# Kernel tuning notes

Hardware: AMD Instinct MI355X
Metric: run time of the kernel (lower is better)

Reference implementation:

```python
import jax, jax.numpy as jnp
import numpy as np


def setup_inputs() -> dict:
    key = jax.random.key(0)
    k0, k1, k2, k3 = jax.random.split(key, 4)
    B, S, D, F, E = 2, 2048, 1024, 4096, 8
    hidden_states = jax.random.normal(k0, (B, S, D), dtype=jnp.float32)
    Wr = jax.random.normal(k1, (E, D), dtype=jnp.float32) * 0.02   # router Linear weight [E, D]
    W1 = jax.random.normal(k2, (E, D, F), dtype=jnp.float32) * 0.02  # expert w1 (transposed torch layout)
    W2 = jax.random.normal(k3, (E, F, D), dtype=jnp.float32) * 0.02  # expert w2
    return {"hidden_states": hidden_states, "Wr": Wr, "W1": W1, "W2": W2, "top_k": 2}


def reference(hidden_states, Wr, W1, W2, top_k):
    # hidden_states: [B, S, D]; Wr: [E, D]; W1: [E, D, F]; W2: [E, F, D]
    E = Wr.shape[0]
    dt = hidden_states.dtype

    # Router: logits -> top-k expert indices. NOTE: the original module computes
    # softmax routing weights over the top-k logits but never applies them in the
    # combine step, so the output is an UNWEIGHTED sum over selected experts.
    router_logits = jnp.einsum('bsd,ed->bse', hidden_states, Wr)
    _, topk_idx = jax.lax.top_k(router_logits, top_k)            # [B, S, K]

    # mask[b,s,e] = 1 if expert e is in token (b,s)'s top-k (indices are distinct)
    mask = (jax.nn.one_hot(topk_idx, E, dtype=dt).sum(axis=-2) > 0).astype(dt)  # [B, S, E]

    # Dense per-expert FFN (SiLU MLP, no bias, dropout=identity in eval):
    h = jax.nn.silu(jnp.einsum('bsd,edf->bsef', hidden_states, W1))  # [B, S, E, F]
    y = jnp.einsum('bsef,efd->bsed', h, W2)                          # [B, S, E, D]

    # Combine: unweighted sum over selected experts (faithful to source)
    return jnp.einsum('bsed,bse->bsd', y, mask)
```

## Files before the change

### kernel.cpp

```cpp
#include <hip/hip_runtime.h>
#include <hip/hip_bf16.h>
#include <stdint.h>

#define TOKENS 4096
#define DDIM 1024
#define FDIM 4096
#define NEXP 8
#define BM 128
#define BN 128
#define BK2 32

typedef __attribute__((ext_vector_type(4))) float f32x4;
typedef __attribute__((ext_vector_type(8))) short short8;

__device__ __forceinline__ unsigned short f2bf(float f) {
    union { float f; uint32_t u; } v; v.f = f;
    uint32_t u = v.u;
    return (unsigned short)((u + 0x7fff + ((u >> 16) & 1)) >> 16);
}

#define BARRIER() asm volatile("s_barrier" ::: "memory")
#define WAIT_VM0() asm volatile("s_waitcnt vmcnt(0)" ::: "memory")
#define WAIT_VM4() asm volatile("s_waitcnt vmcnt(4)" ::: "memory")
#define WAIT_LGKM0() asm volatile("s_waitcnt lgkmcnt(0)" ::: "memory")
#define GLDS(SRC, DST) __builtin_amdgcn_global_load_lds( \
    (const __attribute__((address_space(1))) void*)(SRC), \
    (__attribute__((address_space(3))) void*)(DST), 16, 0, 0)

__device__ __forceinline__ short8 dsr(uint32_t addr) {
    short8 d;
    asm volatile("ds_read_b128 %0, %1" : "=v"(d) : "v"(addr));
    return d;
}

__global__ __launch_bounds__(256) void cvt_x(const float* __restrict__ x,
                                             unsigned short* __restrict__ xb, int n) {
    int i = (blockIdx.x * 256 + threadIdx.x) * 8;
    if (i >= n) return;
    float4 a = *(const float4*)(x + i);
    float4 b = *(const float4*)(x + i + 4);
    short8 o;
    o[0] = f2bf(a.x); o[1] = f2bf(a.y); o[2] = f2bf(a.z); o[3] = f2bf(a.w);
    o[4] = f2bf(b.x); o[5] = f2bf(b.y); o[6] = f2bf(b.z); o[7] = f2bf(b.w);
    *(short8*)(xb + i) = o;
}

__global__ __launch_bounds__(256) void transpose_cvt(const float* __restrict__ in,
                                                     unsigned short* __restrict__ out,
                                                     int R, int C) {
    __shared__ float tile[32][33];
    int e = blockIdx.z;
    int r0 = blockIdx.y * 32, c0 = blockIdx.x * 32;
    const float* src = in + (size_t)e * R * C;
    unsigned short* dst = out + (size_t)e * R * C;
    int t = threadIdx.x;
    int rr = t >> 3;
    int cc = (t & 7) * 4;
    float4 v = *(const float4*)(src + (size_t)(r0 + rr) * C + c0 + cc);
    tile[rr][cc + 0] = v.x; tile[rr][cc + 1] = v.y;
    tile[rr][cc + 2] = v.z; tile[rr][cc + 3] = v.w;
    __syncthreads();
    int oc = rr;
    int orr = cc;
    ushort4 o;
    o.x = f2bf(tile[orr + 0][oc]);
    o.y = f2bf(tile[orr + 1][oc]);
    o.z = f2bf(tile[orr + 2][oc]);
    o.w = f2bf(tile[orr + 3][oc]);
    *(ushort4*)(dst + (size_t)(c0 + oc) * R + r0 + orr) = o;
}

__global__ __launch_bounds__(256) void router(const float* __restrict__ x,
                                              const float* __restrict__ wr,
                                              int* __restrict__ cnt,
                                              int* __restrict__ list) {
    __shared__ float wl[NEXP * DDIM];
    int t = threadIdx.x;
    for (int i = t; i < NEXP * DDIM; i += 256) wl[i] = wr[i];
    __syncthreads();
    int tok = blockIdx.x * 4 + (t >> 6);
    int lane = t & 63;
    float acc[NEXP];
#pragma unroll
    for (int e = 0; e < NEXP; e++) acc[e] = 0.f;
    const float* xr = x + (size_t)tok * DDIM;
    for (int d = lane; d < DDIM; d += 64) {
        float xv = xr[d];
#pragma unroll
        for (int e = 0; e < NEXP; e++) acc[e] += xv * wl[e * DDIM + d];
    }
#pragma unroll
    for (int e = 0; e < NEXP; e++) {
#pragma unroll
        for (int off = 32; off; off >>= 1) acc[e] += __shfl_xor(acc[e], off);
    }
    if (lane == 0) {
        int e1 = 0; float v1 = acc[0];
        for (int e = 1; e < NEXP; e++) if (acc[e] > v1) { v1 = acc[e]; e1 = e; }
        int e2 = -1; float v2 = -1e30f;
        for (int e = 0; e < NEXP; e++) if (e != e1 && acc[e] > v2) { v2 = acc[e]; e2 = e; }
        int p1 = atomicAdd(&cnt[e1], 1);
        list[e1 * TOKENS + p1] = tok;
        int p2 = atomicAdd(&cnt[e2], 1);
        list[e2 * TOKENS + p2] = tok;
    }
}

__global__ void setup(const int* __restrict__ cnt, int* __restrict__ off,
                      int* __restrict__ wbA, int* __restrict__ wbB,
                      int* __restrict__ qctr) {
    if (threadIdx.x == 0) {
        int s = 0, ta = 0, tb = 0;
        for (int e = 0; e < NEXP; e++) {
            off[e] = s; s += cnt[e];
            wbA[e] = ta; wbB[e] = tb;
            int ntm = (cnt[e] + BM - 1) / BM;
            ta += ntm * (FDIM / BN);
            tb += ntm * (DDIM / BN) * 2;
        }
        wbA[NEXP] = ta; wbB[NEXP] = tb;
        qctr[0] = 0; qctr[1] = 0;
    }
}

template <bool GATHER_A, bool SILU, int KSPLIT>
__global__ __launch_bounds__(256, 3) void gemm_moe8(
    const unsigned short* __restrict__ Abase,
    const unsigned short* __restrict__ Wt,
    const int* __restrict__ cnt, const int* __restrict__ off,
    const int* __restrict__ list,
    const int* __restrict__ wbase,
    int* __restrict__ qctr,
    unsigned short* __restrict__ Hout,
    float* __restrict__ Yout,
    int KD, int KLEN, int NW) {
    __shared__ alignas(16) unsigned short As[3][BM * BK2];
    __shared__ alignas(16) unsigned short Bs[3][BN * BK2];
    __shared__ int wsh;

    const int t = threadIdx.x;
    const int lane = t & 63;
    const int wid = t >> 6;
    const int wm = wid >> 1, wn = wid & 1;
    const int r16 = lane & 15, g = lane >> 4;
    const int total = wbase[NEXP];

    const uint32_t asB = (uint32_t)(uintptr_t)&As[0][0];
    const uint32_t bsB = (uint32_t)(uintptr_t)&Bs[0][0];
    uint32_t aAdr[4], bAdr[4];
#pragma unroll
    for (int mi = 0; mi < 4; mi++) {
        int row = wm * 64 + mi * 16 + r16;
        aAdr[mi] = asB + row * 64 + ((g ^ ((row >> 1) & 3)) << 4);
    }
#pragma unroll
    for (int nj = 0; nj < 4; nj++) {
        int row = wn * 64 + nj * 16 + r16;
        bAdr[nj] = bsB + row * 64 + ((g ^ ((row >> 1) & 3)) << 4);
    }

    for (;;) {
        if (t == 0) wsh = atomicAdd(qctr, 1);
        __syncthreads();
        int w = wsh;
        if (w >= total) break;

        int e = 0;
        while (e < NEXP - 1 && w >= wbase[e + 1]) e++;
        w -= wbase[e];
        const int n_e = cnt[e];
        const int ntm = (n_e + BM - 1) >> 7;
        int idx = w / ntm;
        const int mtile = w - idx * ntm;
        int kc = 0;
        if (KSPLIT == 2) { kc = idx & 1; idx >>= 1; }
        const int m0 = mtile * BM;
        const int n0 = idx * BN;
        const int base = off[e];
        const int k0 = kc * KLEN;

        const unsigned short* pA[2];
        const unsigned short* pB[2];
        int ldsOff[2];
#pragma unroll
        for (int i = 0; i < 2; i++) {
            int c = i * 256 + t;
            int row = c >> 2, p = c & 3;
            int cg = p ^ ((row >> 1) & 3);
            int arow = m0 + row; if (arow >= n_e) arow = n_e - 1;
            size_t grow = GATHER_A ? (size_t)list[e * TOKENS + arow] : (size_t)(base + arow);
            pA[i] = Abase + grow * (size_t)KD + k0 + (cg << 3);
            pB[i] = Wt + ((size_t)e * NW + n0 + row) * (size_t)KD + k0 + (cg << 3);
            ldsOff[i] = c * 16;
        }

        f32x4 acc[4][4];
#pragma unroll
        for (int i = 0; i < 4; i++)
#pragma unroll
            for (int j = 0; j < 4; j++) acc[i][j] = f32x4{0.f, 0.f, 0.f, 0.f};

#pragma unroll
        for (int s = 0; s < 2; ++s) {
#pragma unroll
            for (int i = 0; i < 2; i++) { GLDS(pA[i], (char*)As[s] + ldsOff[i]); pA[i] += BK2; }
#pragma unroll
            for (int i = 0; i < 2; i++) { GLDS(pB[i], (char*)Bs[s] + ldsOff[i]); pB[i] += BK2; }
        }
        WAIT_VM4();
        BARRIER();

        uint32_t o0 = 0, o1 = 8192, o2 = 16384;

        const int NT = KLEN / BK2;
        for (int tk = 0; tk < NT; ++tk) {
            if (tk + 2 < NT) {
#pragma unroll
                for (int i = 0; i < 2; i++) { GLDS(pA[i], (char*)As[0] + o2 + ldsOff[i]); pA[i] += BK2; }
#pragma unroll
                for (int i = 0; i < 2; i++) { GLDS(pB[i], (char*)Bs[0] + o2 + ldsOff[i]); pB[i] += BK2; }
            }

            short8 a0 = dsr(aAdr[0] + o0);
            short8 a1 = dsr(aAdr[1] + o0);
            short8 a2 = dsr(aAdr[2] + o0);
            short8 a3 = dsr(aAdr[3] + o0);
            short8 b0 = dsr(bAdr[0] + o0);
            short8 b1 = dsr(bAdr[1] + o0);
            short8 b2 = dsr(bAdr[2] + o0);
            short8 b3 = dsr(bAdr[3] + o0);
            WAIT_LGKM0();
            __builtin_amdgcn_sched_barrier(0);

            __builtin_amdgcn_s_setprio(1);
            acc[0][0] = __builtin_amdgcn_mfma_f32_16x16x32_bf16(a0, b0, acc[0][0], 0, 0, 0);
            acc[0][1] = __builtin_amdgcn_mfma_f32_16x16x32_bf16(a0, b1, acc[0][1], 0, 0, 0);
            acc[0][2] = __builtin_amdgcn_mfma_f32_16x16x32_bf16(a0, b2, acc[0][2], 0, 0, 0);
            acc[0][3] = __builtin_amdgcn_mfma_f32_16x16x32_bf16(a0, b3, acc[0][3], 0, 0, 0);
            acc[1][0] = __builtin_amdgcn_mfma_f32_16x16x32_bf16(a1, b0, acc[1][0], 0, 0, 0);
            acc[1][1] = __builtin_amdgcn_mfma_f32_16x16x32_bf16(a1, b1, acc[1][1], 0, 0, 0);
            acc[1][2] = __builtin_amdgcn_mfma_f32_16x16x32_bf16(a1, b2, acc[1][2], 0, 0, 0);
            acc[1][3] = __builtin_amdgcn_mfma_f32_16x16x32_bf16(a1, b3, acc[1][3], 0, 0, 0);
            acc[2][0] = __builtin_amdgcn_mfma_f32_16x16x32_bf16(a2, b0, acc[2][0], 0, 0, 0);
            acc[2][1] = __builtin_amdgcn_mfma_f32_16x16x32_bf16(a2, b1, acc[2][1], 0, 0, 0);
            acc[2][2] = __builtin_amdgcn_mfma_f32_16x16x32_bf16(a2, b2, acc[2][2], 0, 0, 0);
            acc[2][3] = __builtin_amdgcn_mfma_f32_16x16x32_bf16(a2, b3, acc[2][3], 0, 0, 0);
            acc[3][0] = __builtin_amdgcn_mfma_f32_16x16x32_bf16(a3, b0, acc[3][0], 0, 0, 0);
            acc[3][1] = __builtin_amdgcn_mfma_f32_16x16x32_bf16(a3, b1, acc[3][1], 0, 0, 0);
            acc[3][2] = __builtin_amdgcn_mfma_f32_16x16x32_bf16(a3, b2, acc[3][2], 0, 0, 0);
            acc[3][3] = __builtin_amdgcn_mfma_f32_16x16x32_bf16(a3, b3, acc[3][3], 0, 0, 0);
            __builtin_amdgcn_s_setprio(0);

            if (tk + 1 < NT) {
                if (tk + 2 < NT) WAIT_VM4();
                else             WAIT_VM0();
                BARRIER();
            }
            uint32_t tmp = o0; o0 = o1; o1 = o2; o2 = tmp;
        }

#pragma unroll
        for (int mi = 0; mi < 4; ++mi) {
#pragma unroll
            for (int nj = 0; nj < 4; ++nj) {
#pragma unroll
                for (int qq = 0; qq < 4; ++qq) {
                    int lr = wm * 64 + mi * 16 + g * 4 + qq;
                    if (m0 + lr < n_e) {
                        int col = n0 + wn * 64 + nj * 16 + r16;
                        float v = acc[mi][nj][qq];
                        if (SILU) {
                            v = v / (1.f + __expf(-v));
                            Hout[(size_t)(base + m0 + lr) * NW + col] = f2bf(v);
                        } else {
                            int tok = list[e * TOKENS + m0 + lr];
                            atomicAdd(&Yout[(size_t)tok * NW + col], v);
                        }
                    }
                }
            }
        }
    }
}

extern "C" void kernel_launch(void* const* d_in, const int* in_sizes, int n_in,
                              void* d_out, int out_size, void* d_ws, size_t ws_size,
                              hipStream_t stream) {
    const float* X  = (const float*)d_in[0];
    const float* Wr = (const float*)d_in[1];
    const float* W1 = (const float*)d_in[2];
    const float* W2 = (const float*)d_in[3];
    float* Y = (float*)d_out;

    char* ws = (char*)d_ws;
    int* cnt  = (int*)(ws + 0);
    int* off  = (int*)(ws + 64);
    int* wbA  = (int*)(ws + 128);
    int* wbB  = (int*)(ws + 192);
    int* qctr = (int*)(ws + 256);
    int* list = (int*)(ws + 1024);
    unsigned short* Xb = (unsigned short*)(ws + (1ull << 20));
    unsigned short* WT = (unsigned short*)(ws + (16ull << 20));
    unsigned short* H  = (unsigned short*)(ws + (80ull << 20));

    hipMemsetAsync(d_out, 0, (size_t)out_size * sizeof(float), stream);
    hipMemsetAsync(cnt, 0, 32, stream);

    cvt_x<<<TOKENS * DDIM / (256 * 8), 256, 0, stream>>>(X, Xb, TOKENS * DDIM);
    router<<<TOKENS / 4, 256, 0, stream>>>(X, Wr, cnt, list);
    setup<<<1, 64, 0, stream>>>(cnt, off, wbA, wbB, qctr);

    transpose_cvt<<<dim3(FDIM / 32, DDIM / 32, NEXP), 256, 0, stream>>>(W1, WT, DDIM, FDIM);
    gemm_moe8<true, true, 1><<<768, 256, 0, stream>>>(
        Xb, WT, cnt, off, list, wbA, qctr + 0, H, nullptr, DDIM, DDIM, FDIM);

    transpose_cvt<<<dim3(DDIM / 32, FDIM / 32, NEXP), 256, 0, stream>>>(W2, WT, FDIM, DDIM);
    gemm_moe8<false, false, 2><<<768, 256, 0, stream>>>(
        H, WT, cnt, off, list, wbB, qctr + 1, nullptr, Y, FDIM, FDIM / 2, DDIM);
}
```

Before: 463.1 us.

## Enlarge MoE GEMM tiles to 256x256 with 512-thread blocks and 4-way K split

Doubles the GEMM block tile in both M and N to 256x256, using 8 waves per block, each computing a 128x64 sub-tile with 8x4 MFMA accumulators. The block's A and B tiles are shared across more waves, so the intent is higher arithmetic intensity per LDS and global load. The second GEMM moves from a 2-way to a 4-way K split to keep enough work items. The costs are more registers per wave, fewer resident blocks per CU, more padding waste for expert token counts that are not multiples of 256, and more atomic adds into the output.

```diff
diff --git a/kernel.cpp b/kernel.cpp
--- a/kernel.cpp
+++ b/kernel.cpp
@@ -6,8 +6,8 @@
 #define DDIM 1024
 #define FDIM 4096
 #define NEXP 8
-#define BM 128
-#define BN 128
+#define BM 256
+#define BN 256
 #define BK2 32
 
 typedef __attribute__((ext_vector_type(4))) float f32x4;
@@ -114,9 +114,9 @@
         for (int e = 0; e < NEXP; e++) {
             off[e] = s; s += cnt[e];
             wbA[e] = ta; wbB[e] = tb;
-            int ntm = (cnt[e] + BM - 1) / BM;
+            int ntm = (cnt[e] + BM - 1) >> 8;
             ta += ntm * (FDIM / BN);
-            tb += ntm * (DDIM / BN) * 2;
+            tb += ntm * (DDIM / BN) * 4;
         }
         wbA[NEXP] = ta; wbB[NEXP] = tb;
         qctr[0] = 0; qctr[1] = 0;
@@ -124,7 +124,7 @@
 }
 
 template <bool GATHER_A, bool SILU, int KSPLIT>
-__global__ __launch_bounds__(256, 3) void gemm_moe8(
+__global__ __launch_bounds__(512, 2) void gemm_moe15(
     const unsigned short* __restrict__ Abase,
     const unsigned short* __restrict__ Wt,
     const int* __restrict__ cnt, const int* __restrict__ off,
@@ -141,16 +141,16 @@
     const int t = threadIdx.x;
     const int lane = t & 63;
     const int wid = t >> 6;
-    const int wm = wid >> 1, wn = wid & 1;
+    const int wm = wid >> 2, wn = wid & 3;
     const int r16 = lane & 15, g = lane >> 4;
     const int total = wbase[NEXP];
 
     const uint32_t asB = (uint32_t)(uintptr_t)&As[0][0];
     const uint32_t bsB = (uint32_t)(uintptr_t)&Bs[0][0];
-    uint32_t aAdr[4], bAdr[4];
-#pragma unroll
-    for (int mi = 0; mi < 4; mi++) {
-        int row = wm * 64 + mi * 16 + r16;
+    uint32_t aAdr[8], bAdr[4];
+#pragma unroll
+    for (int mi = 0; mi < 8; mi++) {
+        int row = wm * 128 + mi * 16 + r16;
         aAdr[mi] = asB + row * 64 + ((g ^ ((row >> 1) & 3)) << 4);
     }
 #pragma unroll
@@ -169,11 +169,11 @@
         while (e < NEXP - 1 && w >= wbase[e + 1]) e++;
         w -= wbase[e];
         const int n_e = cnt[e];
-        const int ntm = (n_e + BM - 1) >> 7;
-        int idx = w / ntm;
-        const int mtile = w - idx * ntm;
-        int kc = 0;
-        if (KSPLIT == 2) { kc = idx & 1; idx >>= 1; }
+        const int ntm = (n_e + BM - 1) >> 8;
+        int combined = w / ntm;
+        const int mtile = w - combined * ntm;
+        const int kc = (KSPLIT > 1) ? (combined & (KSPLIT - 1)) : 0;
+        const int idx = (KSPLIT > 1) ? (combined / KSPLIT) : combined;
         const int m0 = mtile * BM;
         const int n0 = idx * BN;
         const int base = off[e];
@@ -184,7 +184,7 @@
         int ldsOff[2];
 #pragma unroll
         for (int i = 0; i < 2; i++) {
-            int c = i * 256 + t;
+            int c = i * 512 + t;
             int row = c >> 2, p = c & 3;
             int cg = p ^ ((row >> 1) & 3);
             int arow = m0 + row; if (arow >= n_e) arow = n_e - 1;
@@ -194,9 +194,9 @@
             ldsOff[i] = c * 16;
         }
 
-        f32x4 acc[4][4];
-#pragma unroll
-        for (int i = 0; i < 4; i++)
+        f32x4 acc[8][4];
+#pragma unroll
+        for (int i = 0; i < 8; i++)
 #pragma unroll
             for (int j = 0; j < 4; j++) acc[i][j] = f32x4{0.f, 0.f, 0.f, 0.f};
 
@@ -210,7 +210,7 @@
         WAIT_VM4();
         BARRIER();
 
-        uint32_t o0 = 0, o1 = 8192, o2 = 16384;
+        uint32_t o0 = 0, o1 = 16384, o2 = 32768;
 
         const int NT = KLEN / BK2;
         for (int tk = 0; tk < NT; ++tk) {
@@ -221,35 +221,63 @@
                 for (int i = 0; i < 2; i++) { GLDS(pB[i], (char*)Bs[0] + o2 + ldsOff[i]); pB[i] += BK2; }
             }
 
-            short8 a0 = dsr(aAdr[0] + o0);
-            short8 a1 = dsr(aAdr[1] + o0);
-            short8 a2 = dsr(aAdr[2] + o0);
-            short8 a3 = dsr(aAdr[3] + o0);
-            short8 b0 = dsr(bAdr[0] + o0);
-            short8 b1 = dsr(bAdr[1] + o0);
-            short8 b2 = dsr(bAdr[2] + o0);
-            short8 b3 = dsr(bAdr[3] + o0);
-            WAIT_LGKM0();
-            __builtin_amdgcn_sched_barrier(0);
-
-            __builtin_amdgcn_s_setprio(1);
-            acc[0][0] = __builtin_amdgcn_mfma_f32_16x16x32_bf16(a0, b0, acc[0][0], 0, 0, 0);
-            acc[0][1] = __builtin_amdgcn_mfma_f32_16x16x32_bf16(a0, b1, acc[0][1], 0, 0, 0);
-            acc[0][2] = __builtin_amdgcn_mfma_f32_16x16x32_bf16(a0, b2, acc[0][2], 0, 0, 0);
-            acc[0][3] = __builtin_amdgcn_mfma_f32_16x16x32_bf16(a0, b3, acc[0][3], 0, 0, 0);
-            acc[1][0] = __builtin_amdgcn_mfma_f32_16x16x32_bf16(a1, b0, acc[1][0], 0, 0, 0);
-            acc[1][1] = __builtin_amdgcn_mfma_f32_16x16x32_bf16(a1, b1, acc[1][1], 0, 0, 0);
-            acc[1][2] = __builtin_amdgcn_mfma_f32_16x16x32_bf16(a1, b2, acc[1][2], 0, 0, 0);
-            acc[1][3] = __builtin_amdgcn_mfma_f32_16x16x32_bf16(a1, b3, acc[1][3], 0, 0, 0);
-            acc[2][0] = __builtin_amdgcn_mfma_f32_16x16x32_bf16(a2, b0, acc[2][0], 0, 0, 0);
-            acc[2][1] = __builtin_amdgcn_mfma_f32_16x16x32_bf16(a2, b1, acc[2][1], 0, 0, 0);
-            acc[2][2] = __builtin_amdgcn_mfma_f32_16x16x32_bf16(a2, b2, acc[2][2], 0, 0, 0);
-            acc[2][3] = __builtin_amdgcn_mfma_f32_16x16x32_bf16(a2, b3, acc[2][3], 0, 0, 0);
-            acc[3][0] = __builtin_amdgcn_mfma_f32_16x16x32_bf16(a3, b0, acc[3][0], 0, 0, 0);
-            acc[3][1] = __builtin_amdgcn_mfma_f32_16x16x32_bf16(a3, b1, acc[3][1], 0, 0, 0);
-            acc[3][2] = __builtin_amdgcn_mfma_f32_16x16x32_bf16(a3, b2, acc[3][2], 0, 0, 0);
-            acc[3][3] = __builtin_amdgcn_mfma_f32_16x16x32_bf16(a3, b3, acc[3][3], 0, 0, 0);
-            __builtin_amdgcn_s_setprio(0);
+            {
+                short8 b0 = dsr(bAdr[0] + o0);
+                short8 b1 = dsr(bAdr[1] + o0);
+                short8 b2 = dsr(bAdr[2] + o0);
+                short8 b3 = dsr(bAdr[3] + o0);
+                short8 a0 = dsr(aAdr[0] + o0);
+                short8 a1 = dsr(aAdr[1] + o0);
+                short8 a2 = dsr(aAdr[2] + o0);
+                short8 a3 = dsr(aAdr[3] + o0);
+                WAIT_LGKM0();
+                __builtin_amdgcn_sched_barrier(0);
+
+                __builtin_amdgcn_s_setprio(1);
+                acc[0][0] = __builtin_amdgcn_mfma_f32_16x16x32_bf16(a0, b0, acc[0][0], 0, 0, 0);
+                acc[0][1] = __builtin_amdgcn_mfma_f32_16x16x32_bf16(a0, b1, acc[0][1], 0, 0, 0);
+                acc[0][2] = __builtin_amdgcn_mfma_f32_16x16x32_bf16(a0, b2, acc[0][2], 0, 0, 0);
+                acc[0][3] = __builtin_amdgcn_mfma_f32_16x16x32_bf16(a0, b3, acc[0][3], 0, 0, 0);
+                acc[1][0] = __builtin_amdgcn_mfma_f32_16x16x32_bf16(a1, b0, acc[1][0], 0, 0, 0);
+                acc[1][1] = __builtin_amdgcn_mfma_f32_16x16x32_bf16(a1, b1, acc[1][1], 0, 0, 0);
+                acc[1][2] = __builtin_amdgcn_mfma_f32_16x16x32_bf16(a1, b2, acc[1][2], 0, 0, 0);
+                acc[1][3] = __builtin_amdgcn_mfma_f32_16x16x32_bf16(a1, b3, acc[1][3], 0, 0, 0);
+                acc[2][0] = __builtin_amdgcn_mfma_f32_16x16x32_bf16(a2, b0, acc[2][0], 0, 0, 0);
+                acc[2][1] = __builtin_amdgcn_mfma_f32_16x16x32_bf16(a2, b1, acc[2][1], 0, 0, 0);
+                acc[2][2] = __builtin_amdgcn_mfma_f32_16x16x32_bf16(a2, b2, acc[2][2], 0, 0, 0);
+                acc[2][3] = __builtin_amdgcn_mfma_f32_16x16x32_bf16(a2, b3, acc[2][3], 0, 0, 0);
+                acc[3][0] = __builtin_amdgcn_mfma_f32_16x16x32_bf16(a3, b0, acc[3][0], 0, 0, 0);
+                acc[3][1] = __builtin_amdgcn_mfma_f32_16x16x32_bf16(a3, b1, acc[3][1], 0, 0, 0);
+                acc[3][2] = __builtin_amdgcn_mfma_f32_16x16x32_bf16(a3, b2, acc[3][2], 0, 0, 0);
+                acc[3][3] = __builtin_amdgcn_mfma_f32_16x16x32_bf16(a3, b3, acc[3][3], 0, 0, 0);
+                __builtin_amdgcn_s_setprio(0);
+
+                short8 a4 = dsr(aAdr[4] + o0);
+                short8 a5 = dsr(aAdr[5] + o0);
+                short8 a6 = dsr(aAdr[6] + o0);
+                short8 a7 = dsr(aAdr[7] + o0);
+                WAIT_LGKM0();
+                __builtin_amdgcn_sched_barrier(0);
+
+                __builtin_amdgcn_s_setprio(1);
+                acc[4][0] = __builtin_amdgcn_mfma_f32_16x16x32_bf16(a4, b0, acc[4][0], 0, 0, 0);
+                acc[4][1] = __builtin_amdgcn_mfma_f32_16x16x32_bf16(a4, b1, acc[4][1], 0, 0, 0);
+                acc[4][2] = __builtin_amdgcn_mfma_f32_16x16x32_bf16(a4, b2, acc[4][2], 0, 0, 0);
+                acc[4][3] = __builtin_amdgcn_mfma_f32_16x16x32_bf16(a4, b3, acc[4][3], 0, 0, 0);
+                acc[5][0] = __builtin_amdgcn_mfma_f32_16x16x32_bf16(a5, b0, acc[5][0], 0, 0, 0);
+                acc[5][1] = __builtin_amdgcn_mfma_f32_16x16x32_bf16(a5, b1, acc[5][1], 0, 0, 0);
+                acc[5][2] = __builtin_amdgcn_mfma_f32_16x16x32_bf16(a5, b2, acc[5][2], 0, 0, 0);
+                acc[5][3] = __builtin_amdgcn_mfma_f32_16x16x32_bf16(a5, b3, acc[5][3], 0, 0, 0);
+                acc[6][0] = __builtin_amdgcn_mfma_f32_16x16x32_bf16(a6, b0, acc[6][0], 0, 0, 0);
+                acc[6][1] = __builtin_amdgcn_mfma_f32_16x16x32_bf16(a6, b1, acc[6][1], 0, 0, 0);
+                acc[6][2] = __builtin_amdgcn_mfma_f32_16x16x32_bf16(a6, b2, acc[6][2], 0, 0, 0);
+                acc[6][3] = __builtin_amdgcn_mfma_f32_16x16x32_bf16(a6, b3, acc[6][3], 0, 0, 0);
+                acc[7][0] = __builtin_amdgcn_mfma_f32_16x16x32_bf16(a7, b0, acc[7][0], 0, 0, 0);
+                acc[7][1] = __builtin_amdgcn_mfma_f32_16x16x32_bf16(a7, b1, acc[7][1], 0, 0, 0);
+                acc[7][2] = __builtin_amdgcn_mfma_f32_16x16x32_bf16(a7, b2, acc[7][2], 0, 0, 0);
+                acc[7][3] = __builtin_amdgcn_mfma_f32_16x16x32_bf16(a7, b3, acc[7][3], 0, 0, 0);
+                __builtin_amdgcn_s_setprio(0);
+            }
 
             if (tk + 1 < NT) {
                 if (tk + 2 < NT) WAIT_VM4();
@@ -260,12 +288,12 @@
         }
 
 #pragma unroll
-        for (int mi = 0; mi < 4; ++mi) {
+        for (int mi = 0; mi < 8; ++mi) {
 #pragma unroll
             for (int nj = 0; nj < 4; ++nj) {
 #pragma unroll
                 for (int qq = 0; qq < 4; ++qq) {
-                    int lr = wm * 64 + mi * 16 + g * 4 + qq;
+                    int lr = wm * 128 + mi * 16 + g * 4 + qq;
                     if (m0 + lr < n_e) {
                         int col = n0 + wn * 64 + nj * 16 + r16;
                         float v = acc[mi][nj][qq];
@@ -311,10 +339,10 @@
     setup<<<1, 64, 0, stream>>>(cnt, off, wbA, wbB, qctr);
 
     transpose_cvt<<<dim3(FDIM / 32, DDIM / 32, NEXP), 256, 0, stream>>>(W1, WT, DDIM, FDIM);
-    gemm_moe8<true, true, 1><<<768, 256, 0, stream>>>(
+    gemm_moe15<true, true, 1><<<256, 512, 0, stream>>>(
         Xb, WT, cnt, off, list, wbA, qctr + 0, H, nullptr, DDIM, DDIM, FDIM);
 
     transpose_cvt<<<dim3(DDIM / 32, FDIM / 32, NEXP), 256, 0, stream>>>(W2, WT, FDIM, DDIM);
-    gemm_moe8<false, false, 2><<<768, 256, 0, stream>>>(
-        H, WT, cnt, off, list, wbB, qctr + 1, nullptr, Y, FDIM, FDIM / 2, DDIM);
-}
+    gemm_moe15<false, false, 4><<<256, 512, 0, stream>>>(
+        H, WT, cnt, off, list, wbB, qctr + 1, nullptr, Y, FDIM, FDIM / 4, DDIM);
+}
```

New measurement: 564.1 us. 1.22x slower.

## Fuse x conversion into router; fold W2 transpose into first GEMM work queue

Applied to the files above, without the earlier changes.

Merges the bf16 conversion of activations into the router kernel so x is read once, and vectorises the router's weight and activation loads. When the workspace is large enough, the W2 transpose/convert is appended as extra work items to the first MoE GEMM's persistent queue and written to a separate buffer. This removes one kernel launch and lets the transpose fill idle GEMM slots. The cost is a larger workspace and transpose tiles competing with GEMM tiles for bandwidth. The unused WAIT_VM8 macro and the kernel rename have no effect.

```diff
diff --git a/kernel.cpp b/kernel.cpp
--- a/kernel.cpp
+++ b/kernel.cpp
@@ -22,6 +22,7 @@
 #define BARRIER() asm volatile("s_barrier" ::: "memory")
 #define WAIT_VM0() asm volatile("s_waitcnt vmcnt(0)" ::: "memory")
 #define WAIT_VM4() asm volatile("s_waitcnt vmcnt(4)" ::: "memory")
+#define WAIT_VM8() asm volatile("s_waitcnt vmcnt(8)" ::: "memory")
 #define WAIT_LGKM0() asm volatile("s_waitcnt lgkmcnt(0)" ::: "memory")
 #define GLDS(SRC, DST) __builtin_amdgcn_global_load_lds( \
     (const __attribute__((address_space(1))) void*)(SRC), \
@@ -31,18 +32,6 @@
     short8 d;
     asm volatile("ds_read_b128 %0, %1" : "=v"(d) : "v"(addr));
     return d;
-}
-
-__global__ __launch_bounds__(256) void cvt_x(const float* __restrict__ x,
-                                             unsigned short* __restrict__ xb, int n) {
-    int i = (blockIdx.x * 256 + threadIdx.x) * 8;
-    if (i >= n) return;
-    float4 a = *(const float4*)(x + i);
-    float4 b = *(const float4*)(x + i + 4);
-    short8 o;
-    o[0] = f2bf(a.x); o[1] = f2bf(a.y); o[2] = f2bf(a.z); o[3] = f2bf(a.w);
-    o[4] = f2bf(b.x); o[5] = f2bf(b.y); o[6] = f2bf(b.z); o[7] = f2bf(b.w);
-    *(short8*)(xb + i) = o;
 }
 
 __global__ __launch_bounds__(256) void transpose_cvt(const float* __restrict__ in,
@@ -70,13 +59,15 @@
     *(ushort4*)(dst + (size_t)(c0 + oc) * R + r0 + orr) = o;
 }
 
-__global__ __launch_bounds__(256) void router(const float* __restrict__ x,
-                                              const float* __restrict__ wr,
-                                              int* __restrict__ cnt,
-                                              int* __restrict__ list) {
+__global__ __launch_bounds__(256) void router_cvt(const float* __restrict__ x,
+                                                  const float* __restrict__ wr,
+                                                  unsigned short* __restrict__ xb,
+                                                  int* __restrict__ cnt,
+                                                  int* __restrict__ list) {
     __shared__ float wl[NEXP * DDIM];
     int t = threadIdx.x;
-    for (int i = t; i < NEXP * DDIM; i += 256) wl[i] = wr[i];
+    for (int i = t * 4; i < NEXP * DDIM; i += 256 * 4)
+        *(float4*)&wl[i] = *(const float4*)&wr[i];
     __syncthreads();
     int tok = blockIdx.x * 4 + (t >> 6);
     int lane = t & 63;
@@ -84,10 +75,19 @@
 #pragma unroll
     for (int e = 0; e < NEXP; e++) acc[e] = 0.f;
     const float* xr = x + (size_t)tok * DDIM;
-    for (int d = lane; d < DDIM; d += 64) {
-        float xv = xr[d];
-#pragma unroll
-        for (int e = 0; e < NEXP; e++) acc[e] += xv * wl[e * DDIM + d];
+    unsigned short* xbr = xb + (size_t)tok * DDIM;
+#pragma unroll
+    for (int c = 0; c < 4; c++) {
+        int d = c * 256 + lane * 4;
+        float4 v = *(const float4*)(xr + d);
+        ushort4 o;
+        o.x = f2bf(v.x); o.y = f2bf(v.y); o.z = f2bf(v.z); o.w = f2bf(v.w);
+        *(ushort4*)(xbr + d) = o;
+#pragma unroll
+        for (int e = 0; e < NEXP; e++) {
+            float4 w4 = *(const float4*)&wl[e * DDIM + d];
+            acc[e] += v.x * w4.x + v.y * w4.y + v.z * w4.z + v.w * w4.w;
+        }
     }
 #pragma unroll
     for (int e = 0; e < NEXP; e++) {
@@ -124,7 +124,7 @@
 }
 
 template <bool GATHER_A, bool SILU, int KSPLIT>
-__global__ __launch_bounds__(256, 3) void gemm_moe8(
+__global__ __launch_bounds__(256, 3) void gemm_moe16(
     const unsigned short* __restrict__ Abase,
     const unsigned short* __restrict__ Wt,
     const int* __restrict__ cnt, const int* __restrict__ off,
@@ -133,6 +133,9 @@
     int* __restrict__ qctr,
     unsigned short* __restrict__ Hout,
     float* __restrict__ Yout,
+    const float* __restrict__ TRsrc,
+    unsigned short* __restrict__ TRdst,
+    int extra,
     int KD, int KLEN, int NW) {
     __shared__ alignas(16) unsigned short As[3][BM * BK2];
     __shared__ alignas(16) unsigned short Bs[3][BN * BK2];
@@ -144,6 +147,7 @@
     const int wm = wid >> 1, wn = wid & 1;
     const int r16 = lane & 15, g = lane >> 4;
     const int total = wbase[NEXP];
+    const int totalAll = total + extra;
 
     const uint32_t asB = (uint32_t)(uintptr_t)&As[0][0];
     const uint32_t bsB = (uint32_t)(uintptr_t)&Bs[0][0];
@@ -163,7 +167,32 @@
         if (t == 0) wsh = atomicAdd(qctr, 1);
         __syncthreads();
         int w = wsh;
-        if (w >= total) break;
+        if (w >= totalAll) break;
+
+        if (w >= total) {
+            int tr = w - total;
+            int e = tr >> 7;
+            int f0 = (tr & 127) << 5;
+            const float* src = TRsrc + (size_t)e * FDIM * DDIM;
+            unsigned short* dst = TRdst + (size_t)e * FDIM * DDIM;
+            float* tile = (float*)&As[0][0];
+            int rr = t >> 3;
+            int cc = (t & 7) * 4;
+            for (int c0 = 0; c0 < DDIM; c0 += 32) {
+                float4 v = *(const float4*)(src + (size_t)(f0 + rr) * DDIM + c0 + cc);
+                tile[rr * 33 + cc + 0] = v.x; tile[rr * 33 + cc + 1] = v.y;
+                tile[rr * 33 + cc + 2] = v.z; tile[rr * 33 + cc + 3] = v.w;
+                __syncthreads();
+                ushort4 o;
+                o.x = f2bf(tile[(cc + 0) * 33 + rr]);
+                o.y = f2bf(tile[(cc + 1) * 33 + rr]);
+                o.z = f2bf(tile[(cc + 2) * 33 + rr]);
+                o.w = f2bf(tile[(cc + 3) * 33 + rr]);
+                *(ushort4*)(dst + (size_t)(c0 + rr) * FDIM + f0 + cc) = o;
+                __syncthreads();
+            }
+            continue;
+        }
 
         int e = 0;
         while (e < NEXP - 1 && w >= wbase[e + 1]) e++;
@@ -299,22 +328,31 @@
     int* wbB  = (int*)(ws + 192);
     int* qctr = (int*)(ws + 256);
     int* list = (int*)(ws + 1024);
-    unsigned short* Xb = (unsigned short*)(ws + (1ull << 20));
-    unsigned short* WT = (unsigned short*)(ws + (16ull << 20));
-    unsigned short* H  = (unsigned short*)(ws + (80ull << 20));
+    unsigned short* Xb  = (unsigned short*)(ws + (1ull << 20));
+    unsigned short* WT1 = (unsigned short*)(ws + (16ull << 20));
+    unsigned short* H   = (unsigned short*)(ws + (80ull << 20));
+
+    const bool fuse = ws_size >= (208ull << 20);
+    unsigned short* WT2 = fuse ? (unsigned short*)(ws + (144ull << 20)) : WT1;
+    const int extraA = fuse ? NEXP * (FDIM / 32) : 0;
 
     hipMemsetAsync(d_out, 0, (size_t)out_size * sizeof(float), stream);
     hipMemsetAsync(cnt, 0, 32, stream);
 
-    cvt_x<<<TOKENS * DDIM / (256 * 8), 256, 0, stream>>>(X, Xb, TOKENS * DDIM);
-    router<<<TOKENS / 4, 256, 0, stream>>>(X, Wr, cnt, list);
+    router_cvt<<<TOKENS / 4, 256, 0, stream>>>(X, Wr, Xb, cnt, list);
     setup<<<1, 64, 0, stream>>>(cnt, off, wbA, wbB, qctr);
 
-    transpose_cvt<<<dim3(FDIM / 32, DDIM / 32, NEXP), 256, 0, stream>>>(W1, WT, DDIM, FDIM);
-    gemm_moe8<true, true, 1><<<768, 256, 0, stream>>>(
-        Xb, WT, cnt, off, list, wbA, qctr + 0, H, nullptr, DDIM, DDIM, FDIM);
-
-    transpose_cvt<<<dim3(DDIM / 32, FDIM / 32, NEXP), 256, 0, stream>>>(W2, WT, FDIM, DDIM);
-    gemm_moe8<false, false, 2><<<768, 256, 0, stream>>>(
-        H, WT, cnt, off, list, wbB, qctr + 1, nullptr, Y, FDIM, FDIM / 2, DDIM);
-}
+    transpose_cvt<<<dim3(FDIM / 32, DDIM / 32, NEXP), 256, 0, stream>>>(W1, WT1, DDIM, FDIM);
+
+    gemm_moe16<true, true, 1><<<768, 256, 0, stream>>>(
+        Xb, WT1, cnt, off, list, wbA, qctr + 0, H, nullptr,
+        W2, WT2, extraA, DDIM, DDIM, FDIM);
+
+    if (!fuse) {
+        transpose_cvt<<<dim3(DDIM / 32, FDIM / 32, NEXP), 256, 0, stream>>>(W2, WT2, FDIM, DDIM);
+    }
+
+    gemm_moe16<false, false, 2><<<768, 256, 0, stream>>>(
+        H, WT2, cnt, off, list, wbB, qctr + 1, nullptr, Y,
+        nullptr, nullptr, 0, FDIM, FDIM / 2, DDIM);
+}
```

Result: slower. 480.1 us (+3.7%).
